# Kernel optimization log

Measured on AMD Instinct MI355X. Metric: run time of the kernel, lower is better.

The kernel has to match this reference:

```python
import jax, jax.numpy as jnp
import numpy as np

B, IN, OUT, R, G = 1024, 4096, 4096, 16, 16
N_GROUPS = IN * OUT // G  # 1048576


def setup_inputs() -> dict:
    key = jax.random.key(0)
    k1, k2, k3, k4, k5 = jax.random.split(key, 5)
    x = jax.random.normal(k1, (B, IN), dtype=jnp.float32)
    # packed 4-bit weights: each int holds two nibbles (low | high<<4), values 0..255
    qweight = jax.random.randint(k2, (N_GROUPS, G // 2), 0, 256, dtype=jnp.int32)
    # positive per-group scale (original stores abs-max as fp16, used as fp32)
    scale_factor = jax.random.uniform(k3, (N_GROUPS, 1), dtype=jnp.float32, minval=0.01, maxval=1.0)
    # kaiming-normal-ish init for lora_a; lora_b nonzero for a non-degenerate baseline
    lora_a = jax.random.normal(k4, (R, IN), dtype=jnp.float32) * np.sqrt(2.0 / IN).astype(np.float32)
    lora_b = jax.random.normal(k5, (OUT, R), dtype=jnp.float32) * 0.01
    alpha = jnp.ones((1,), dtype=jnp.float32)
    return {"x": x, "qweight": qweight, "scale_factor": scale_factor,
            "lora_a": lora_a, "lora_b": lora_b, "alpha": alpha}


def _dequantize_4bit(qweight, scale_factor):
    # qweight: [n_groups, G/2] int32 packed nibbles; scale: [n_groups, 1]
    g, half = qweight.shape
    lo = qweight & 15            # even positions
    hi = (qweight >> 4) & 15     # odd positions
    q8 = jnp.stack([lo, hi], axis=-1).reshape(g, half * 2)  # interleave -> [n_groups, G]
    x_norm = q8.astype(jnp.float32) / 15.0
    return x_norm * 2.0 * scale_factor - scale_factor       # [n_groups, G]


def reference(x, qweight, scale_factor, lora_a, lora_b, alpha):
    # dequantize and view as (in_features, -1), matching weight.view(x.shape[1], -1)
    weight = _dequantize_4bit(qweight, scale_factor).reshape(x.shape[1], -1)  # [IN, OUT]
    base = jnp.einsum('bi,oi->bo', x, weight)  # F.linear(x, weight) = x @ weight.T
    lora = alpha * jnp.einsum('br,or->bo', jnp.einsum('bi,ri->br', x, lora_a), lora_b)
    return base + lora
```

## Files before the change

### kernel.cpp

```cpp
#include <hip/hip_runtime.h>

typedef __attribute__((ext_vector_type(2))) _Float16 h2;
typedef __attribute__((ext_vector_type(2))) __fp16 p2;
typedef __attribute__((ext_vector_type(8))) _Float16 f16x8;
typedef __attribute__((ext_vector_type(4))) float fv4;
typedef __attribute__((ext_vector_type(4))) int iv4;
typedef unsigned int u32;

#define K_IN 4096
#define N_OUT 4096
#define KE 4160

__global__ __launch_bounds__(256) void xa_kernel(const float* __restrict__ x,
                                                 const float* __restrict__ la,
                                                 float* __restrict__ xa) {
    int b = blockIdx.x;
    int t = threadIdx.x;
    const fv4* xp = (const fv4*)(x + (size_t)b * K_IN);
    fv4 xv[4];
#pragma unroll
    for (int j = 0; j < 4; ++j) xv[j] = xp[t + j * 256];
    float acc[16];
#pragma unroll
    for (int r = 0; r < 16; ++r) {
        const fv4* ap = (const fv4*)(la + (size_t)r * K_IN);
        float s = 0.f;
#pragma unroll
        for (int j = 0; j < 4; ++j) {
            fv4 av = ap[t + j * 256];
            s = fmaf(xv[j].x, av.x, s);
            s = fmaf(xv[j].y, av.y, s);
            s = fmaf(xv[j].z, av.z, s);
            s = fmaf(xv[j].w, av.w, s);
        }
        acc[r] = s;
    }
#pragma unroll
    for (int r = 0; r < 16; ++r) {
#pragma unroll
        for (int off = 1; off < 64; off <<= 1)
            acc[r] += __shfl_xor(acc[r], off);
    }
    __shared__ float red[4][16];
    int lane = t & 63, w = t >> 6;
    if (lane < 16) red[w][lane] = acc[lane];
    __syncthreads();
    if (t < 16) xa[b * 16 + t] = red[0][t] + red[1][t] + red[2][t] + red[3][t];
}

__global__ __launch_bounds__(256) void w_dequant(const int* __restrict__ qw,
                                                 const float* __restrict__ sc,
                                                 _Float16* __restrict__ Wh) {
    int grp = blockIdx.x * 256 + threadIdx.x;
    int o = grp >> 8;
    int i0 = (grp & 255) << 4;
    const int* qp = qw + (size_t)grp * 8;
    iv4 q0 = *(const iv4*)qp;
    iv4 q1 = *(const iv4*)(qp + 4);
    float s = sc[grp];
    _Float16 c0h = (_Float16)(s * (2.0f / 15.0f));
    _Float16 c1h = (_Float16)(-s);
    h2 c0 = {c0h, c0h}, c1 = {c1h, c1h};
    h2 m1024 = {(_Float16)-1024.f, (_Float16)-1024.f};
    union { h2 h[4]; iv4 v; } o0, o1;
    int vals[8] = {q0.x, q0.y, q0.z, q0.w, q1.x, q1.y, q1.z, q1.w};
#pragma unroll
    for (int e = 0; e < 8; ++e) {
        unsigned wv = (unsigned)vals[e];
        unsigned qb = (wv & 15u) | ((wv & 0xF0u) << 12) | 0x64006400u;
        h2 qh;
        __builtin_memcpy(&qh, &qb, 4);
        h2 r = (qh + m1024) * c0 + c1;
        if (e < 4) o0.h[e] = r; else o1.h[e - 4] = r;
    }
    _Float16* wp = Wh + (size_t)o * KE + i0;
    *(iv4*)(wp) = o0.v;
    *(iv4*)(wp + 8) = o1.v;
}

__global__ __launch_bounds__(256) void w_pad(const float* __restrict__ lb,
                                             const float* __restrict__ alphap,
                                             _Float16* __restrict__ Wh) {
    int c = blockIdx.x * 256 + threadIdx.x;
    int o = c >> 3, j = c & 7;
    union { p2 h[4]; iv4 v; } u;
    u.v = iv4{0, 0, 0, 0};
    if (j < 2) {
        float al = alphap[0];
        const float* wp = lb + (size_t)o * 16 + j * 8;
#pragma unroll
        for (int e = 0; e < 4; ++e)
            u.h[e] = __builtin_amdgcn_cvt_pkrtz(al * wp[2 * e], al * wp[2 * e + 1]);
    }
    *(iv4*)(Wh + (size_t)o * KE + 4096 + j * 8) = u.v;
}

__global__ __launch_bounds__(256) void x_build(const float* __restrict__ x,
                                               const float* __restrict__ xa,
                                               _Float16* __restrict__ xh) {
    int c = blockIdx.x * 256 + threadIdx.x;
    int b = (int)((unsigned)c / 520u);
    int col8 = c - b * 520;
    union { p2 h[4]; iv4 v; } u;
    if (col8 < 512) {
        const float* p = x + (size_t)b * K_IN + col8 * 8;
        fv4 v0 = *(const fv4*)(p);
        fv4 v1 = *(const fv4*)(p + 4);
        u.h[0] = __builtin_amdgcn_cvt_pkrtz(v0.x, v0.y);
        u.h[1] = __builtin_amdgcn_cvt_pkrtz(v0.z, v0.w);
        u.h[2] = __builtin_amdgcn_cvt_pkrtz(v1.x, v1.y);
        u.h[3] = __builtin_amdgcn_cvt_pkrtz(v1.z, v1.w);
    } else if (col8 < 514) {
        const float* p = xa + (size_t)b * 16 + (col8 - 512) * 8;
        fv4 v0 = *(const fv4*)(p);
        fv4 v1 = *(const fv4*)(p + 4);
        u.h[0] = __builtin_amdgcn_cvt_pkrtz(v0.x, v0.y);
        u.h[1] = __builtin_amdgcn_cvt_pkrtz(v0.z, v0.w);
        u.h[2] = __builtin_amdgcn_cvt_pkrtz(v1.x, v1.y);
        u.h[3] = __builtin_amdgcn_cvt_pkrtz(v1.z, v1.w);
    } else {
        u.v = iv4{0, 0, 0, 0};
    }
    *(iv4*)(xh + (size_t)b * KE + col8 * 8) = u.v;
}

__global__ __launch_bounds__(512, 1) void qlora_gemm2(
        const _Float16* __restrict__ xh, const _Float16* __restrict__ Wh,
        float* __restrict__ out)
{
    __shared__ __align__(16) char lds[98304];

    int bid = blockIdx.x;
    int by = bid & 7, bx = bid >> 3;
    int bm0 = by << 7, bn0 = bx << 7;

    int t = threadIdx.x;
    int lane = t & 63;
    int wid = t >> 6;
    int kg = wid & 1, wn = (wid >> 1) & 1, wm = wid >> 2;
    int rl = lane & 15, hq = lane >> 4;

    int srow = t >> 3;
    int slg = t & 7;
    int sg = slg ^ (srow & 7);
    const char* a0 = (const char*)(xh + (size_t)(bm0 + srow) * KE) + sg * 16;
    const char* a1 = (const char*)(xh + (size_t)(bm0 + srow + 64) * KE) + sg * 16;
    const char* b0 = (const char*)(Wh + (size_t)(bn0 + srow) * KE) + sg * 16;
    const char* b1 = (const char*)(Wh + (size_t)(bn0 + srow + 64) * KE) + sg * 16;

    auto GLOAD = [&](int ts, int buf) {
        char* Ad = lds + buf * 16384;
        char* Bd = lds + 49152 + buf * 16384;
        size_t off = (size_t)ts * 128;
        __builtin_amdgcn_global_load_lds(
            (const __attribute__((address_space(1))) u32*)(a0 + off),
            (__attribute__((address_space(3))) u32*)(Ad + t * 16), 16, 0, 0);
        __builtin_amdgcn_global_load_lds(
            (const __attribute__((address_space(1))) u32*)(a1 + off),
            (__attribute__((address_space(3))) u32*)(Ad + 8192 + t * 16), 16, 0, 0);
        __builtin_amdgcn_global_load_lds(
            (const __attribute__((address_space(1))) u32*)(b0 + off),
            (__attribute__((address_space(3))) u32*)(Bd + t * 16), 16, 0, 0);
        __builtin_amdgcn_global_load_lds(
            (const __attribute__((address_space(1))) u32*)(b1 + off),
            (__attribute__((address_space(3))) u32*)(Bd + 8192 + t * 16), 16, 0, 0);
    };

    fv4 acc[4][4];
#pragma unroll
    for (int m = 0; m < 4; ++m)
#pragma unroll
        for (int n = 0; n < 4; ++n)
            acc[m][n] = fv4{0.f, 0.f, 0.f, 0.f};

    auto COMPUTE = [&](int buf) {
        const char* As = lds + buf * 16384;
        const char* Bs = lds + 49152 + buf * 16384;
        f16x8 a[4], b[4];
        int gk = kg * 4 + hq;
        int gs = (gk ^ (rl & 7)) << 4;
#pragma unroll
        for (int m = 0; m < 4; ++m)
            a[m] = *(const f16x8*)(As + (wm * 64 + m * 16 + rl) * 128 + gs);
#pragma unroll
        for (int n = 0; n < 4; ++n)
            b[n] = *(const f16x8*)(Bs + (wn * 64 + n * 16 + rl) * 128 + gs);
        __builtin_amdgcn_s_setprio(1);
#pragma unroll
        for (int m = 0; m < 4; ++m)
#pragma unroll
            for (int n = 0; n < 4; ++n)
                acc[m][n] = __builtin_amdgcn_mfma_f32_16x16x32_f16(
                    a[m], b[n], acc[m][n], 0, 0, 0);
        __builtin_amdgcn_s_setprio(0);
    };

    GLOAD(0, 0);
    GLOAD(1, 1);
    asm volatile("s_waitcnt vmcnt(4)" ::: "memory");
    __builtin_amdgcn_s_barrier();
    __builtin_amdgcn_sched_barrier(0);

#pragma unroll 1
    for (int ts = 0; ts < 65; ++ts) {
        if (ts + 2 < 65) GLOAD(ts + 2, (ts + 2) % 3);
        COMPUTE(ts % 3);
        if (ts + 2 < 65)
            asm volatile("s_waitcnt vmcnt(4)" ::: "memory");
        else
            asm volatile("s_waitcnt vmcnt(0)" ::: "memory");
        __builtin_amdgcn_s_barrier();
        __builtin_amdgcn_sched_barrier(0);
    }

    if (kg == 1) {
        char* dmp = lds + (wm * 2 + wn) * 16384;
#pragma unroll
        for (int m = 0; m < 4; ++m)
#pragma unroll
            for (int n = 0; n < 4; ++n)
                *(fv4*)(dmp + (m * 4 + n) * 1024 + lane * 16) = acc[m][n];
    }
    __syncthreads();
    if (kg == 0) {
        const char* dmp = lds + (wm * 2 + wn) * 16384;
#pragma unroll
        for (int m = 0; m < 4; ++m) {
            int row0 = bm0 + wm * 64 + m * 16 + hq * 4;
#pragma unroll
            for (int n = 0; n < 4; ++n) {
                fv4 p = *(const fv4*)(dmp + (m * 4 + n) * 1024 + lane * 16);
                fv4 v = acc[m][n];
                v.x += p.x; v.y += p.y; v.z += p.z; v.w += p.w;
                int col = bn0 + wn * 64 + n * 16 + rl;
#pragma unroll
                for (int r = 0; r < 4; ++r)
                    out[(size_t)(row0 + r) * N_OUT + col] = v[r];
            }
        }
    }
}

extern "C" void kernel_launch(void* const* d_in, const int* in_sizes, int n_in,
                              void* d_out, int out_size, void* d_ws, size_t ws_size,
                              hipStream_t stream) {
    const float* x  = (const float*)d_in[0];
    const int*   qw = (const int*)d_in[1];
    const float* sc = (const float*)d_in[2];
    const float* la = (const float*)d_in[3];
    const float* lb = (const float*)d_in[4];
    const float* al = (const float*)d_in[5];
    float* out = (float*)d_out;

    const size_t WH_BYTES = (size_t)N_OUT * KE * 2;
    const size_t XH_BYTES = (size_t)1024 * KE * 2;
    const size_t XA_BYTES = (size_t)1024 * 16 * 4;

    _Float16* Wh = (_Float16*)d_ws;
    _Float16* xh = (_Float16*)((char*)d_ws + WH_BYTES);
    float*    xa = (float*)((char*)d_ws + WH_BYTES + XH_BYTES);
    (void)ws_size; (void)n_in; (void)in_sizes; (void)out_size;
    (void)XA_BYTES;

    xa_kernel<<<1024, 256, 0, stream>>>(x, la, xa);
    w_dequant<<<4096, 256, 0, stream>>>(qw, sc, Wh);
    w_pad<<<128, 256, 0, stream>>>(lb, al, Wh);
    x_build<<<2080, 256, 0, stream>>>(x, xa, xh);
    qlora_gemm2<<<256, 512, 0, stream>>>(xh, Wh, out);
}
```

Measured before the change: 84.68 us.

## Fuse prep kernels and switch GEMM to 256-wide K tiles with XCD remap

The xa computation and fp16 conversion of x move into one x_prep kernel, and weight dequant plus the LoRA-B padding are merged into one launch, cutting five launches to three and dropping an intermediate buffer round-trip. The GEMM switches from a 3-stage 128-wide K pipeline to a 2-stage 256-wide K pipeline with 128KB LDS, a 16-way swizzle, and a separate tail step for the 64-column LoRA extension. Block indices are remapped so each XCD handles a contiguous group of N tiles, which should improve L2 reuse. The shallower pipeline waits on vmcnt(0) every iteration, which may expose load latency.

```diff
diff --git a/kernel.cpp b/kernel.cpp
--- a/kernel.cpp
+++ b/kernel.cpp
@@ -5,21 +5,30 @@
 typedef __attribute__((ext_vector_type(8))) _Float16 f16x8;
 typedef __attribute__((ext_vector_type(4))) float fv4;
 typedef __attribute__((ext_vector_type(4))) int iv4;
+typedef __attribute__((ext_vector_type(2))) int iv2;
 typedef unsigned int u32;
 
 #define K_IN 4096
 #define N_OUT 4096
 #define KE 4160
 
-__global__ __launch_bounds__(256) void xa_kernel(const float* __restrict__ x,
-                                                 const float* __restrict__ la,
-                                                 float* __restrict__ xa) {
+__global__ __launch_bounds__(256) void x_prep(const float* __restrict__ x,
+                                              const float* __restrict__ la,
+                                              _Float16* __restrict__ xh) {
     int b = blockIdx.x;
     int t = threadIdx.x;
     const fv4* xp = (const fv4*)(x + (size_t)b * K_IN);
+    _Float16* xr = xh + (size_t)b * KE;
     fv4 xv[4];
 #pragma unroll
     for (int j = 0; j < 4; ++j) xv[j] = xp[t + j * 256];
+#pragma unroll
+    for (int j = 0; j < 4; ++j) {
+        union { p2 h[2]; iv2 v; } u;
+        u.h[0] = __builtin_amdgcn_cvt_pkrtz(xv[j].x, xv[j].y);
+        u.h[1] = __builtin_amdgcn_cvt_pkrtz(xv[j].z, xv[j].w);
+        *(iv2*)(xr + (size_t)(t + j * 256) * 4) = u.v;
+    }
     float acc[16];
 #pragma unroll
     for (int r = 0; r < 16; ++r) {
@@ -45,93 +54,70 @@
     int lane = t & 63, w = t >> 6;
     if (lane < 16) red[w][lane] = acc[lane];
     __syncthreads();
-    if (t < 16) xa[b * 16 + t] = red[0][t] + red[1][t] + red[2][t] + red[3][t];
-}
-
-__global__ __launch_bounds__(256) void w_dequant(const int* __restrict__ qw,
-                                                 const float* __restrict__ sc,
-                                                 _Float16* __restrict__ Wh) {
-    int grp = blockIdx.x * 256 + threadIdx.x;
-    int o = grp >> 8;
-    int i0 = (grp & 255) << 4;
-    const int* qp = qw + (size_t)grp * 8;
-    iv4 q0 = *(const iv4*)qp;
-    iv4 q1 = *(const iv4*)(qp + 4);
-    float s = sc[grp];
-    _Float16 c0h = (_Float16)(s * (2.0f / 15.0f));
-    _Float16 c1h = (_Float16)(-s);
-    h2 c0 = {c0h, c0h}, c1 = {c1h, c1h};
-    h2 m1024 = {(_Float16)-1024.f, (_Float16)-1024.f};
-    union { h2 h[4]; iv4 v; } o0, o1;
-    int vals[8] = {q0.x, q0.y, q0.z, q0.w, q1.x, q1.y, q1.z, q1.w};
-#pragma unroll
-    for (int e = 0; e < 8; ++e) {
-        unsigned wv = (unsigned)vals[e];
-        unsigned qb = (wv & 15u) | ((wv & 0xF0u) << 12) | 0x64006400u;
-        h2 qh;
-        __builtin_memcpy(&qh, &qb, 4);
-        h2 r = (qh + m1024) * c0 + c1;
-        if (e < 4) o0.h[e] = r; else o1.h[e - 4] = r;
-    }
-    _Float16* wp = Wh + (size_t)o * KE + i0;
-    *(iv4*)(wp) = o0.v;
-    *(iv4*)(wp + 8) = o1.v;
-}
-
-__global__ __launch_bounds__(256) void w_pad(const float* __restrict__ lb,
-                                             const float* __restrict__ alphap,
-                                             _Float16* __restrict__ Wh) {
-    int c = blockIdx.x * 256 + threadIdx.x;
-    int o = c >> 3, j = c & 7;
-    union { p2 h[4]; iv4 v; } u;
-    u.v = iv4{0, 0, 0, 0};
-    if (j < 2) {
-        float al = alphap[0];
-        const float* wp = lb + (size_t)o * 16 + j * 8;
-#pragma unroll
-        for (int e = 0; e < 4; ++e)
-            u.h[e] = __builtin_amdgcn_cvt_pkrtz(al * wp[2 * e], al * wp[2 * e + 1]);
-    }
-    *(iv4*)(Wh + (size_t)o * KE + 4096 + j * 8) = u.v;
-}
-
-__global__ __launch_bounds__(256) void x_build(const float* __restrict__ x,
-                                               const float* __restrict__ xa,
-                                               _Float16* __restrict__ xh) {
-    int c = blockIdx.x * 256 + threadIdx.x;
-    int b = (int)((unsigned)c / 520u);
-    int col8 = c - b * 520;
-    union { p2 h[4]; iv4 v; } u;
-    if (col8 < 512) {
-        const float* p = x + (size_t)b * K_IN + col8 * 8;
-        fv4 v0 = *(const fv4*)(p);
-        fv4 v1 = *(const fv4*)(p + 4);
-        u.h[0] = __builtin_amdgcn_cvt_pkrtz(v0.x, v0.y);
-        u.h[1] = __builtin_amdgcn_cvt_pkrtz(v0.z, v0.w);
-        u.h[2] = __builtin_amdgcn_cvt_pkrtz(v1.x, v1.y);
-        u.h[3] = __builtin_amdgcn_cvt_pkrtz(v1.z, v1.w);
-    } else if (col8 < 514) {
-        const float* p = xa + (size_t)b * 16 + (col8 - 512) * 8;
-        fv4 v0 = *(const fv4*)(p);
-        fv4 v1 = *(const fv4*)(p + 4);
-        u.h[0] = __builtin_amdgcn_cvt_pkrtz(v0.x, v0.y);
-        u.h[1] = __builtin_amdgcn_cvt_pkrtz(v0.z, v0.w);
-        u.h[2] = __builtin_amdgcn_cvt_pkrtz(v1.x, v1.y);
-        u.h[3] = __builtin_amdgcn_cvt_pkrtz(v1.z, v1.w);
+    if (t < 16)
+        xr[4096 + t] = (_Float16)(red[0][t] + red[1][t] + red[2][t] + red[3][t]);
+    else if (t < 64)
+        xr[4112 + (t - 16)] = (_Float16)0.f;
+}
+
+__global__ __launch_bounds__(256) void w_dequant2(const int* __restrict__ qw,
+                                                  const float* __restrict__ sc,
+                                                  const float* __restrict__ lb,
+                                                  const float* __restrict__ alphap,
+                                                  _Float16* __restrict__ Wh) {
+    int bid = blockIdx.x;
+    int t = threadIdx.x;
+    if (bid < 4096) {
+        int grp = bid * 256 + t;
+        int o = grp >> 8;
+        int i0 = (grp & 255) << 4;
+        const int* qp = qw + (size_t)grp * 8;
+        iv4 q0 = *(const iv4*)qp;
+        iv4 q1 = *(const iv4*)(qp + 4);
+        float s = sc[grp];
+        _Float16 c0h = (_Float16)(s * (2.0f / 15.0f));
+        _Float16 c1h = (_Float16)(-s);
+        h2 c0 = {c0h, c0h}, c1 = {c1h, c1h};
+        h2 m1024 = {(_Float16)-1024.f, (_Float16)-1024.f};
+        union { h2 h[4]; iv4 v; } o0, o1;
+        int vals[8] = {q0.x, q0.y, q0.z, q0.w, q1.x, q1.y, q1.z, q1.w};
+#pragma unroll
+        for (int e = 0; e < 8; ++e) {
+            unsigned wv = (unsigned)vals[e];
+            unsigned qb = (wv & 15u) | ((wv & 0xF0u) << 12) | 0x64006400u;
+            h2 qh;
+            __builtin_memcpy(&qh, &qb, 4);
+            h2 r = (qh + m1024) * c0 + c1;
+            if (e < 4) o0.h[e] = r; else o1.h[e - 4] = r;
+        }
+        _Float16* wp = Wh + (size_t)o * KE + i0;
+        *(iv4*)(wp) = o0.v;
+        *(iv4*)(wp + 8) = o1.v;
     } else {
+        int c = (bid - 4096) * 256 + t;
+        int o = c >> 3, jj = c & 7;
+        union { p2 h[4]; iv4 v; } u;
         u.v = iv4{0, 0, 0, 0};
-    }
-    *(iv4*)(xh + (size_t)b * KE + col8 * 8) = u.v;
+        if (jj < 2) {
+            float al = alphap[0];
+            const float* wp = lb + (size_t)o * 16 + jj * 8;
+#pragma unroll
+            for (int e = 0; e < 4; ++e)
+                u.h[e] = __builtin_amdgcn_cvt_pkrtz(al * wp[2 * e], al * wp[2 * e + 1]);
+        }
+        *(iv4*)(Wh + (size_t)o * KE + 4096 + jj * 8) = u.v;
+    }
 }
 
 __global__ __launch_bounds__(512, 1) void qlora_gemm2(
         const _Float16* __restrict__ xh, const _Float16* __restrict__ Wh,
         float* __restrict__ out)
 {
-    __shared__ __align__(16) char lds[98304];
+    __shared__ __align__(16) char lds[131072];
 
     int bid = blockIdx.x;
-    int by = bid & 7, bx = bid >> 3;
+    int xcd = bid & 7, j = bid >> 3;
+    int by = j & 7, bx = xcd * 4 + (j >> 3);
     int bm0 = by << 7, bn0 = bx << 7;
 
     int t = threadIdx.x;
@@ -140,30 +126,52 @@
     int kg = wid & 1, wn = (wid >> 1) & 1, wm = wid >> 2;
     int rl = lane & 15, hq = lane >> 4;
 
-    int srow = t >> 3;
-    int slg = t & 7;
-    int sg = slg ^ (srow & 7);
-    const char* a0 = (const char*)(xh + (size_t)(bm0 + srow) * KE) + sg * 16;
-    const char* a1 = (const char*)(xh + (size_t)(bm0 + srow + 64) * KE) + sg * 16;
-    const char* b0 = (const char*)(Wh + (size_t)(bn0 + srow) * KE) + sg * 16;
-    const char* b1 = (const char*)(Wh + (size_t)(bn0 + srow + 64) * KE) + sg * 16;
+    int sr = t >> 4;
+    int sp = t & 15;
+    int sg = sp ^ (sr & 15);
+    const char* asrc[4];
+    const char* bsrc[4];
+#pragma unroll
+    for (int i = 0; i < 4; ++i) {
+        asrc[i] = (const char*)(xh + (size_t)(bm0 + i * 32 + sr) * KE) + sg * 16;
+        bsrc[i] = (const char*)(Wh + (size_t)(bn0 + i * 32 + sr) * KE) + sg * 16;
+    }
+    int tr = t >> 3;
+    int tg = (t & 7) ^ (tr & 7);
+    const char* atail[2];
+    const char* btail[2];
+#pragma unroll
+    for (int i = 0; i < 2; ++i) {
+        atail[i] = (const char*)(xh + (size_t)(bm0 + i * 64 + tr) * KE + 4096) + tg * 16;
+        btail[i] = (const char*)(Wh + (size_t)(bn0 + i * 64 + tr) * KE + 4096) + tg * 16;
+    }
 
     auto GLOAD = [&](int ts, int buf) {
-        char* Ad = lds + buf * 16384;
-        char* Bd = lds + 49152 + buf * 16384;
-        size_t off = (size_t)ts * 128;
-        __builtin_amdgcn_global_load_lds(
-            (const __attribute__((address_space(1))) u32*)(a0 + off),
-            (__attribute__((address_space(3))) u32*)(Ad + t * 16), 16, 0, 0);
-        __builtin_amdgcn_global_load_lds(
-            (const __attribute__((address_space(1))) u32*)(a1 + off),
-            (__attribute__((address_space(3))) u32*)(Ad + 8192 + t * 16), 16, 0, 0);
-        __builtin_amdgcn_global_load_lds(
-            (const __attribute__((address_space(1))) u32*)(b0 + off),
-            (__attribute__((address_space(3))) u32*)(Bd + t * 16), 16, 0, 0);
-        __builtin_amdgcn_global_load_lds(
-            (const __attribute__((address_space(1))) u32*)(b1 + off),
-            (__attribute__((address_space(3))) u32*)(Bd + 8192 + t * 16), 16, 0, 0);
+        char* Ad = lds + buf * 32768;
+        char* Bd = lds + 65536 + buf * 32768;
+        size_t off = (size_t)ts * 256;
+#pragma unroll
+        for (int i = 0; i < 4; ++i) {
+            __builtin_amdgcn_global_load_lds(
+                (const __attribute__((address_space(1))) u32*)(asrc[i] + off),
+                (__attribute__((address_space(3))) u32*)(Ad + i * 8192 + t * 16), 16, 0, 0);
+            __builtin_amdgcn_global_load_lds(
+                (const __attribute__((address_space(1))) u32*)(bsrc[i] + off),
+                (__attribute__((address_space(3))) u32*)(Bd + i * 8192 + t * 16), 16, 0, 0);
+        }
+    };
+    auto GLOAD_TAIL = [&](int buf) {
+        char* Ad = lds + buf * 32768;
+        char* Bd = lds + 65536 + buf * 32768;
+#pragma unroll
+        for (int i = 0; i < 2; ++i) {
+            __builtin_amdgcn_global_load_lds(
+                (const __attribute__((address_space(1))) u32*)(atail[i]),
+                (__attribute__((address_space(3))) u32*)(Ad + i * 8192 + t * 16), 16, 0, 0);
+            __builtin_amdgcn_global_load_lds(
+                (const __attribute__((address_space(1))) u32*)(btail[i]),
+                (__attribute__((address_space(3))) u32*)(Bd + i * 8192 + t * 16), 16, 0, 0);
+        }
     };
 
     fv4 acc[4][4];
@@ -174,8 +182,32 @@
             acc[m][n] = fv4{0.f, 0.f, 0.f, 0.f};
 
     auto COMPUTE = [&](int buf) {
-        const char* As = lds + buf * 16384;
-        const char* Bs = lds + 49152 + buf * 16384;
+        const char* As = lds + buf * 32768;
+        const char* Bs = lds + 65536 + buf * 32768;
+#pragma unroll
+        for (int s = 0; s < 2; ++s) {
+            f16x8 a[4], b[4];
+            int gk = kg * 8 + s * 4 + hq;
+            int gs = (gk ^ rl) << 4;
+#pragma unroll
+            for (int m = 0; m < 4; ++m)
+                a[m] = *(const f16x8*)(As + (wm * 64 + m * 16 + rl) * 256 + gs);
+#pragma unroll
+            for (int n = 0; n < 4; ++n)
+                b[n] = *(const f16x8*)(Bs + (wn * 64 + n * 16 + rl) * 256 + gs);
+            __builtin_amdgcn_s_setprio(1);
+#pragma unroll
+            for (int m = 0; m < 4; ++m)
+#pragma unroll
+                for (int n = 0; n < 4; ++n)
+                    acc[m][n] = __builtin_amdgcn_mfma_f32_16x16x32_f16(
+                        a[m], b[n], acc[m][n], 0, 0, 0);
+            __builtin_amdgcn_s_setprio(0);
+        }
+    };
+    auto COMPUTE_TAIL = [&](int buf) {
+        const char* As = lds + buf * 32768;
+        const char* Bs = lds + 65536 + buf * 32768;
         f16x8 a[4], b[4];
         int gk = kg * 4 + hq;
         int gs = (gk ^ (rl & 7)) << 4;
@@ -196,23 +228,22 @@
     };
 
     GLOAD(0, 0);
-    GLOAD(1, 1);
-    asm volatile("s_waitcnt vmcnt(4)" ::: "memory");
+    asm volatile("s_waitcnt vmcnt(0)" ::: "memory");
     __builtin_amdgcn_s_barrier();
     __builtin_amdgcn_sched_barrier(0);
 
 #pragma unroll 1
-    for (int ts = 0; ts < 65; ++ts) {
-        if (ts + 2 < 65) GLOAD(ts + 2, (ts + 2) % 3);
-        COMPUTE(ts % 3);
-        if (ts + 2 < 65)
-            asm volatile("s_waitcnt vmcnt(4)" ::: "memory");
-        else
-            asm volatile("s_waitcnt vmcnt(0)" ::: "memory");
+    for (int ts = 0; ts < 32; ++ts) {
+        if (ts < 31) GLOAD(ts + 1, (ts + 1) & 1);
+        else         GLOAD_TAIL(0);
+        COMPUTE(ts & 1);
+        asm volatile("s_waitcnt vmcnt(0) lgkmcnt(0)" ::: "memory");
         __builtin_amdgcn_s_barrier();
         __builtin_amdgcn_sched_barrier(0);
     }
-
+    COMPUTE_TAIL(0);
+
+    __syncthreads();
     if (kg == 1) {
         char* dmp = lds + (wm * 2 + wn) * 16384;
 #pragma unroll
@@ -253,18 +284,11 @@
     float* out = (float*)d_out;
 
     const size_t WH_BYTES = (size_t)N_OUT * KE * 2;
-    const size_t XH_BYTES = (size_t)1024 * KE * 2;
-    const size_t XA_BYTES = (size_t)1024 * 16 * 4;
-
     _Float16* Wh = (_Float16*)d_ws;
     _Float16* xh = (_Float16*)((char*)d_ws + WH_BYTES);
-    float*    xa = (float*)((char*)d_ws + WH_BYTES + XH_BYTES);
     (void)ws_size; (void)n_in; (void)in_sizes; (void)out_size;
-    (void)XA_BYTES;
-
-    xa_kernel<<<1024, 256, 0, stream>>>(x, la, xa);
-    w_dequant<<<4096, 256, 0, stream>>>(qw, sc, Wh);
-    w_pad<<<128, 256, 0, stream>>>(lb, al, Wh);
-    x_build<<<2080, 256, 0, stream>>>(x, xa, xh);
+
+    x_prep<<<1024, 256, 0, stream>>>(x, la, xh);
+    w_dequant2<<<4224, 256, 0, stream>>>(qw, sc, lb, al, Wh);
     qlora_gemm2<<<256, 512, 0, stream>>>(xh, Wh, out);
 }
```

New measurement: 73.13 us. 1.16x faster.
